# Kernel optimization log

Measured on AMD Instinct MI355X. Metric: run time of the kernel, lower is better.

Reference implementation:

```python
import jax, jax.numpy as jnp
import numpy as np

B, C, T = 8, 512, 4096
KC, VC, H = 512, 512, 1  # key_channels, value_channels, num_heads
SCALE = KC // (H ** 0.5)  # faithful to original: key_channels // num_heads**0.5


def setup_inputs() -> dict:
    key = jax.random.key(0)
    k1, k2, k3, k4, k5 = jax.random.split(key, 5)
    x = jax.random.normal(k1, (B, C, T), dtype=jnp.float32)
    # 1x1 Conv1d weights: Conv1d(C, out, kernel_size=1) == per-timestep Linear
    Wqk = jax.random.normal(k2, (KC, C), dtype=jnp.float32) / np.sqrt(C)
    bqk = jax.random.normal(k3, (KC,), dtype=jnp.float32) * 0.01
    Wv = jax.random.normal(k4, (VC, C), dtype=jnp.float32) / np.sqrt(C)
    bv = jax.random.normal(k5, (VC,), dtype=jnp.float32) * 0.01
    return {"x": x, "Wqk": Wqk, "bqk": bqk, "Wv": Wv, "bv": bv}


def reference(x, Wqk, bqk, Wv, bv):
    # 1x1 conv projections: [B,C,T] -> [B,K,T] / [B,V,T]
    qk = jnp.einsum('kc,bct->bkt', Wqk, x) + bqk[None, :, None]
    val = jnp.einsum('vc,bct->bvt', Wv, x) + bv[None, :, None]
    # channel-wise attention: with num_heads=1 the reshape/transpose/matmul
    # chain reduces to scores[b,k,v] = sum_t qk[b,k,t] * val[b,v,t]
    scores = jnp.einsum('bkt,bvt->bkv', qk, val) / SCALE
    p = jax.nn.softmax(scores, axis=-1)          # softmax over value channels
    # inference path: dropout is identity (self.training == False)
    out = jnp.einsum('bkv,bvt->bkt', p, val)     # [B,K,T], K == input_channels
    return out.reshape(-1, C, T)
```

## Files before the change

kernel.cpp:

```cpp
#include <hip/hip_runtime.h>
#include <hip/hip_bf16.h>


#define BB 8
#define CC 512
#define TT 4096

typedef __attribute__((ext_vector_type(8))) short bf16x8;
typedef __attribute__((ext_vector_type(4))) short bf16x4;
typedef __attribute__((ext_vector_type(4))) float f32x4;

__device__ __forceinline__ void gload_lds16(const void* g, void* l) {
  __builtin_amdgcn_global_load_lds((const __attribute__((address_space(1))) void*)g,
                                   (__attribute__((address_space(3))) void*)l,
                                   16, 0, 0);
}
__device__ __forceinline__ float bf2f(short u) {
  return __uint_as_float(((unsigned)(unsigned short)u) << 16);
}
__device__ __forceinline__ unsigned short f2bf(float f) {
  return __builtin_bit_cast(unsigned short, __float2bfloat16(f));
}
__device__ __forceinline__ void bar_fence() {
  asm volatile("" ::: "memory");
  __builtin_amdgcn_s_barrier();
  asm volatile("" ::: "memory");
}
__device__ __forceinline__ void bar_lds() {
  asm volatile("s_waitcnt lgkmcnt(0)" ::: "memory");
  __builtin_amdgcn_s_barrier();
  asm volatile("" ::: "memory");
}

__global__ __launch_bounds__(256)
void convert_stream_kernel(const float* __restrict__ x, __hip_bfloat16* __restrict__ xh,
                           float* __restrict__ sx)
{
  const int gid = blockIdx.x * 256 + threadIdx.x;
#pragma unroll
  for (int it = 0; it < 4; it++) {
    const int chunk = it * 524288 + gid;
    const size_t base = (size_t)chunk * 8;
    const float4 a = *(const float4*)&x[base];
    const float4 c = *(const float4*)&x[base + 4];
    bf16x8 h;
    h[0] = (short)f2bf(a.x); h[1] = (short)f2bf(a.y);
    h[2] = (short)f2bf(a.z); h[3] = (short)f2bf(a.w);
    h[4] = (short)f2bf(c.x); h[5] = (short)f2bf(c.y);
    h[6] = (short)f2bf(c.z); h[7] = (short)f2bf(c.w);
    *(bf16x8*)&xh[base] = h;
    float s = ((a.x + a.y) + (a.z + a.w)) + ((c.x + c.y) + (c.z + c.w));
#pragma unroll
    for (int off = 32; off; off >>= 1) s += __shfl_xor(s, off);
    if ((threadIdx.x & 63) == 0) atomicAdd(&sx[chunk >> 9], s);
  }
}

__global__ __launch_bounds__(256)
void prep_w_kernel(const float* __restrict__ Wqk, const float* __restrict__ Wv,
                   const float* __restrict__ sx,
                   __hip_bfloat16* __restrict__ Wqkh, __hip_bfloat16* __restrict__ Wvh,
                   __hip_bfloat16* __restrict__ WvT,
                   float* __restrict__ ta, float* __restrict__ tb)
{
  const int blk = blockIdx.x;
  if (blk < 1024) {
    int i = blk * 256 + threadIdx.x;
    Wqkh[i] = __float2bfloat16(Wqk[i]);
    float wv = Wv[i];
    Wvh[i] = __float2bfloat16(wv);
    WvT[(i & 511) * 512 + (i >> 9)] = __float2bfloat16(wv);
  } else {
    int wid = threadIdx.x >> 6, lane = threadIdx.x & 63;
    int gid = (blk - 1024) * 4 + wid;
    int which = gid >> 12;
    int rem = gid & 4095;
    int b = rem >> 9, j = rem & 511;
    const float* W = which ? Wv : Wqk;
    float s = 0.f;
#pragma unroll
    for (int i2 = 0; i2 < 8; i2++) {
      int c = lane + i2 * 64;
      s += W[j * 512 + c] * sx[b * 512 + c];
    }
#pragma unroll
    for (int off = 32; off; off >>= 1) s += __shfl_xor(s, off);
    if (lane == 0) (which ? tb : ta)[b * 512 + j] = s;
  }
}

template <int BM, int BN>
__global__ __launch_bounds__(256)
void gemm_nt_kernel(const __hip_bfloat16* __restrict__ A, long strideA, int ldA,
                    const __hip_bfloat16* __restrict__ B, long strideB, int ldB,
                    void* __restrict__ C, long strideC, int ldC,
                    int Kslice, int nslices)
{
  static_assert(BM == 128 && BN == 128, "vmcnt(8) count assumes 8 loads/stage");
  constexpr int FM = BM / 32, FN = BN / 32;
  const int tid = threadIdx.x, lane = tid & 63, wid = tid >> 6;

  const int gx = gridDim.x, gy = gridDim.y;
  const int lin = blockIdx.x + gx * (blockIdx.y + gy * blockIdx.z);
  const int nwg = gx * gy * (int)gridDim.z;
  const int lin2 = (lin & 7) * (nwg >> 3) + (lin >> 3);
  const int tn = lin2 % gx;
  const int r1 = lin2 / gx;
  const int tm = r1 % gy;
  const int z  = r1 / gy;
  const int b  = z / nslices;
  const int ks = z - b * nslices;

  const __hip_bfloat16* Ab = A + (size_t)b * strideA + (size_t)(tm * BM) * ldA + (size_t)ks * Kslice;
  const __hip_bfloat16* Bb = B + (size_t)b * strideB + (size_t)(tn * BN) * ldB + (size_t)ks * Kslice;

  __shared__ __align__(16) __hip_bfloat16 sA[2][BM * 64];
  __shared__ __align__(16) __hip_bfloat16 sB[2][BN * 64];

  const int wr = wid >> 1, wc = wid & 1;

  f32x4 acc[FM][FN];
#pragma unroll
  for (int m = 0; m < FM; m++)
#pragma unroll
    for (int n = 0; n < FN; n++) acc[m][n] = (f32x4){0.f, 0.f, 0.f, 0.f};

  auto stage = [&](int buf, int k0) {
#pragma unroll
    for (int i = 0; i < BM / 32; i++) {
      int e = tid * 8 + i * 2048;
      int row = e >> 6, colg = (e & 63) ^ ((row & 7) << 3);
      gload_lds16(Ab + (size_t)row * ldA + k0 + colg, &sA[buf][wid * 512 + i * 2048]);
    }
#pragma unroll
    for (int i = 0; i < BN / 32; i++) {
      int e = tid * 8 + i * 2048;
      int row = e >> 6, colg = (e & 63) ^ ((row & 7) << 3);
      gload_lds16(Bb + (size_t)row * ldB + k0 + colg, &sB[buf][wid * 512 + i * 2048]);
    }
  };

  const int nsteps = Kslice >> 6;
  stage(0, 0);
  if (nsteps > 1) stage(1, 64);
#pragma unroll 1
  for (int s = 0; s < nsteps; s++) {
    if (s + 1 < nsteps) asm volatile("s_waitcnt vmcnt(8)" ::: "memory");
    else                asm volatile("s_waitcnt vmcnt(0)" ::: "memory");
    bar_fence();
    const __hip_bfloat16* cA = sA[s & 1];
    const __hip_bfloat16* cB = sB[s & 1];
#pragma unroll
    for (int ks2 = 0; ks2 < 2; ks2++) {
      bf16x8 af[FM], bfv[FN];
      const int kb = ks2 * 32 + (lane >> 4) * 8;
#pragma unroll
      for (int m = 0; m < FM; m++) {
        int row = wr * (BM / 2) + m * 16 + (lane & 15);
        af[m] = *(const bf16x8*)&cA[row * 64 + (kb ^ ((row & 7) << 3))];
      }
#pragma unroll
      for (int n = 0; n < FN; n++) {
        int row = wc * (BN / 2) + n * 16 + (lane & 15);
        bfv[n] = *(const bf16x8*)&cB[row * 64 + (kb ^ ((row & 7) << 3))];
      }
#pragma unroll
      for (int m = 0; m < FM; m++)
#pragma unroll
        for (int n = 0; n < FN; n++)
          acc[m][n] = __builtin_amdgcn_mfma_f32_16x16x32_bf16(af[m], bfv[n], acc[m][n], 0, 0, 0);
    }
    bar_fence();
    if (s + 2 < nsteps) stage(s & 1, (s + 2) << 6);
  }

  const int rb = tm * BM + wr * (BM / 2) + ((lane >> 4) << 2);
  const int cb = tn * BN + wc * (BN / 2) + (lane & 15);
  __hip_bfloat16* Cb = (__hip_bfloat16*)C + (size_t)z * strideC;
#pragma unroll
  for (int m = 0; m < FM; m++)
#pragma unroll
    for (int n = 0; n < FN; n++)
#pragma unroll
      for (int r = 0; r < 4; r++) {
        int row = rb + m * 16 + r, col = cb + n * 16;
        Cb[(size_t)row * ldC + col] = __float2bfloat16(acc[m][n][r]);
      }
}

__global__ __launch_bounds__(256)
void reduce_g_kernel(const short* __restrict__ Gpart, short* __restrict__ Gb)
{
  const int idx = (blockIdx.x * 256 + threadIdx.x) * 8;
  const int b = idx >> 18, i = idx & 262143;
  const short* base = Gpart + ((size_t)(b * 4) << 18) + i;
  float s[8];
#pragma unroll
  for (int q = 0; q < 8; q++) s[q] = 0.f;
#pragma unroll
  for (int ks = 0; ks < 4; ks++) {
    bf16x8 v = *(const bf16x8*)(base + ((size_t)ks << 18));
#pragma unroll
    for (int q = 0; q < 8; q++) s[q] += bf2f(v[q]);
  }
  bf16x8 o;
#pragma unroll
  for (int q = 0; q < 8; q++) o[q] = (short)f2bf(s[q]);
  *(bf16x8*)(Gb + ((size_t)b << 18) + i) = o;
}

__global__ __launch_bounds__(256)
void middle_kernel(const __hip_bfloat16* __restrict__ Gh,
                   const __hip_bfloat16* __restrict__ Wqkh,
                   const __hip_bfloat16* __restrict__ Wvh,
                   const __hip_bfloat16* __restrict__ WvT,
                   const float* __restrict__ bqk, const float* __restrict__ bv,
                   const float* __restrict__ ta, const float* __restrict__ tb,
                   __hip_bfloat16* __restrict__ Mm, float* __restrict__ pb)
{
  __shared__ __align__(16) __hip_bfloat16 sW[16 * 512];
  __shared__ __align__(16) __hip_bfloat16 sT[16 * 512];
  __shared__ __align__(16) __hip_bfloat16 sB[2][512 * 32];
  __shared__ float red1[4][16], red2[4][16], red3[4][16];

  const int tid = threadIdx.x, lane = tid & 63, wid = tid >> 6;
  const int lin = blockIdx.x;
  const int lin2 = (lin & 7) * 32 + (lin >> 3);
  const int strip = lin2 & 31, b = lin2 >> 5;
  const __hip_bfloat16* Ghb = Gh + (size_t)b * 262144;

#pragma unroll
  for (int i = 0; i < 4; i++) {
    int row = i * 4 + wid;
    int scol = 8 * (lane ^ (row & 7));
    gload_lds16(Wqkh + (size_t)(strip * 16 + row) * 512 + scol, &sW[i * 2048 + wid * 512]);
  }

  auto stageB = [&](int buf, int gt) {
    const __hip_bfloat16* Bsrc = (gt < 16) ? Ghb : (gt < 32 ? Wvh : WvT);
    const int k0 = (gt & 15) * 32;
#pragma unroll
    for (int i = 0; i < 8; i++) {
      int r = i * 64 + wid * 16 + (lane >> 2);
      int scol = k0 + 8 * ((lane & 3) ^ ((r >> 1) & 3));
      gload_lds16(Bsrc + (size_t)r * 512 + scol, &sB[buf][i * 2048 + wid * 512]);
    }
  };

  stageB(0, 0);
  stageB(1, 1);

  const int arow = lane & 15;
  const int asw = (arow & 7) << 3;
  const int kb = (lane >> 4) * 8;
  f32x4 acc[8];

  auto run16 = [&](int base, const __hip_bfloat16* SX) {
#pragma unroll
    for (int n = 0; n < 8; n++) acc[n] = (f32x4){0.f, 0.f, 0.f, 0.f};
#pragma unroll 1
    for (int t = 0; t < 16; t++) {
      const int gt = base + t;
      if (gt + 1 < 48) asm volatile("s_waitcnt vmcnt(8)" ::: "memory");
      else             asm volatile("s_waitcnt vmcnt(0)" ::: "memory");
      bar_fence();
      const __hip_bfloat16* cB = sB[gt & 1];
      const int kq = t * 32 + kb;
      bf16x8 af = *(const bf16x8*)&SX[arow * 512 + (kq ^ asw)];
#pragma unroll
      for (int n = 0; n < 8; n++) {
        int brow = wid * 128 + n * 16 + (lane & 15);
        bf16x8 bfv = *(const bf16x8*)&cB[brow * 32 + (kb ^ (((brow >> 1) & 3) << 3))];
        acc[n] = __builtin_amdgcn_mfma_f32_16x16x32_bf16(af, bfv, acc[n], 0, 0, 0);
      }
      bar_fence();
      if (gt + 2 < 48) stageB(gt & 1, gt + 2);
    }
  };

  run16(0, sW);
#pragma unroll
  for (int n = 0; n < 8; n++)
#pragma unroll
    for (int r = 0; r < 4; r++) {
      int lr = ((lane >> 4) << 2) + r;
      int col = wid * 128 + n * 16 + (lane & 15);
      sT[lr * 512 + (col ^ ((lr & 7) << 3))] = __float2bfloat16(acc[n][r]);
    }
  bar_lds();

  run16(16, sT);

  const float* tab = ta + b * 512;
  const float* tbb = tb + b * 512;
  float bvc[8], tbc[8];
#pragma unroll
  for (int n = 0; n < 8; n++) {
    int col = wid * 128 + n * 16 + (lane & 15);
    bvc[n] = bv[col]; tbc[n] = tbb[col];
  }
  float bq[4], tar[4];
#pragma unroll
  for (int r = 0; r < 4; r++) {
    int gr = strip * 16 + ((lane >> 4) << 2) + r;
    bq[r] = bqk[gr]; tar[r] = tab[gr];
  }
#pragma unroll
  for (int n = 0; n < 8; n++)
#pragma unroll
    for (int r = 0; r < 4; r++)
      acc[n][r] = (acc[n][r] + bq[r] * tbc[n] + tar[r] * bvc[n]
                   + 4096.0f * bq[r] * bvc[n]) * (1.0f / 512.0f);

#pragma unroll
  for (int r = 0; r < 4; r++) {
    float v = acc[0][r];
#pragma unroll
    for (int n = 1; n < 8; n++) v = fmaxf(v, acc[n][r]);
#pragma unroll
    for (int off = 1; off < 16; off <<= 1) v = fmaxf(v, __shfl_xor(v, off));
    if ((lane & 15) == 0) red1[wid][((lane >> 4) << 2) + r] = v;
  }
  bar_lds();
  float mx[4];
#pragma unroll
  for (int r = 0; r < 4; r++) {
    int lr = ((lane >> 4) << 2) + r;
    mx[r] = fmaxf(fmaxf(red1[0][lr], red1[1][lr]), fmaxf(red1[2][lr], red1[3][lr]));
  }
#pragma unroll
  for (int r = 0; r < 4; r++) {
    float s = 0.f, pp = 0.f;
#pragma unroll
    for (int n = 0; n < 8; n++) {
      float e = __expf(acc[n][r] - mx[r]);
      acc[n][r] = e;
      s += e; pp += e * bvc[n];
    }
#pragma unroll
    for (int off = 1; off < 16; off <<= 1) { s += __shfl_xor(s, off); pp += __shfl_xor(pp, off); }
    if ((lane & 15) == 0) {
      red2[wid][((lane >> 4) << 2) + r] = s;
      red3[wid][((lane >> 4) << 2) + r] = pp;
    }
  }
  bar_lds();
  float inv[4];
#pragma unroll
  for (int r = 0; r < 4; r++) {
    int lr = ((lane >> 4) << 2) + r;
    float sum = red2[0][lr] + red2[1][lr] + red2[2][lr] + red2[3][lr];
    inv[r] = 1.0f / sum;
    if (wid == 0 && (lane & 15) == 0)
      pb[b * 512 + strip * 16 + lr] =
          (red3[0][lr] + red3[1][lr] + red3[2][lr] + red3[3][lr]) * inv[r];
  }
#pragma unroll
  for (int n = 0; n < 8; n++)
#pragma unroll
    for (int r = 0; r < 4; r++) {
      int lr = ((lane >> 4) << 2) + r;
      int col = wid * 128 + n * 16 + (lane & 15);
      sT[lr * 512 + (col ^ ((lr & 7) << 3))] = __float2bfloat16(acc[n][r] * inv[r]);
    }
  bar_lds();

  run16(32, sT);

  __hip_bfloat16* Mb = Mm + (size_t)b * 262144 + (size_t)(strip * 16) * 512;
#pragma unroll
  for (int n = 0; n < 8; n++)
#pragma unroll
    for (int r = 0; r < 4; r++) {
      int lr = ((lane >> 4) << 2) + r;
      int col = wid * 128 + n * 16 + (lane & 15);
      Mb[(size_t)lr * 512 + col] = __float2bfloat16(acc[n][r]);
    }
}

__global__ __launch_bounds__(256)
void gemm_out_kernel(const __hip_bfloat16* __restrict__ Mall,
                     const __hip_bfloat16* __restrict__ xh,
                     const float* __restrict__ pball,
                     float* __restrict__ out)
{
  __shared__ __align__(16) __hip_bfloat16 sA[2][128 * 64];
  __shared__ __align__(16) __hip_bfloat16 sB[2][64 * 128];

  const int tid = threadIdx.x, lane = tid & 63, wid = tid >> 6;
  const int wr = wid >> 1, wc = wid & 1;

  const int lin = blockIdx.x + 32 * (blockIdx.y + 4 * blockIdx.z);
  const int lin2 = (lin & 7) * 128 + (lin >> 3);
  const int tm = lin2 & 3;
  const int tn = (lin2 >> 2) & 31;
  const int b  = lin2 >> 7;

  const __hip_bfloat16* Ab = Mall + (size_t)b * 262144 + (size_t)(tm * 128) * 512;
  const __hip_bfloat16* Bb = xh + (size_t)b * ((size_t)CC * TT) + tn * 128;

  f32x4 acc[4][4];
#pragma unroll
  for (int m = 0; m < 4; m++)
#pragma unroll
    for (int n = 0; n < 4; n++) acc[m][n] = (f32x4){0.f, 0.f, 0.f, 0.f};

  auto stage = [&](int buf, int k0) {
#pragma unroll
    for (int i = 0; i < 4; i++) {
      int e = tid * 8 + i * 2048;
      int row = e >> 6, colg = (e & 63) ^ ((row & 7) << 3);
      gload_lds16(Ab + (size_t)row * 512 + k0 + colg, &sA[buf][wid * 512 + i * 2048]);
    }
#pragma unroll
    for (int q = 0; q < 4; q++) {
      int E = q * 2048 + tid * 8;
      int v = ((E >> 9) << 2) | ((E >> 4) & 3);
      int t = (((E >> 6) & 7) << 4) | (E & 8);
      gload_lds16(Bb + (size_t)(k0 + v) * TT + t, &sB[buf][wid * 512 + q * 2048]);
    }
  };

  const unsigned sB32 =
      (unsigned)(size_t)(__attribute__((address_space(3))) __hip_bfloat16*)&sB[0][0];
  const unsigned btr_lo = sB32 + (lane >> 4) * 2048 + (lane & 15) * 8 + wc * 512;
  const unsigned btr_hi = btr_lo + 8192;

#define COMPUTE(BUF)                                                            \
  {                                                                             \
    _Pragma("unroll")                                                           \
    for (int ks2 = 0; ks2 < 2; ks2++) {                                         \
      bf16x8 af[4]; bf16x4 blo[4], bhi[4];                                      \
      const int kb = ks2 * 32 + (lane >> 4) * 8;                                \
      _Pragma("unroll")                                                         \
      for (int m = 0; m < 4; m++) {                                             \
        int row = wr * 64 + m * 16 + (lane & 15);                               \
        af[m] = *(const bf16x8*)&sA[BUF][row * 64 + (kb ^ ((row & 7) << 3))];   \
      }                                                                         \
      unsigned ab = ks2 ? btr_hi : btr_lo;                                      \
      _Pragma("unroll")                                                         \
      for (int n = 0; n < 4; n++) {                                             \
        asm volatile("ds_read_b64_tr_b16 %0, %1 offset:%2"                      \
                     : "=v"(blo[n]) : "v"(ab), "i"((BUF) * 16384 + n * 128));   \
        asm volatile("ds_read_b64_tr_b16 %0, %1 offset:%2"                      \
                     : "=v"(bhi[n]) : "v"(ab), "i"((BUF) * 16384 + n * 128 + 1024)); \
      }                                                                         \
      asm volatile("s_waitcnt lgkmcnt(0)" ::: "memory");                        \
      __builtin_amdgcn_sched_barrier(0);                                        \
      _Pragma("unroll")                                                         \
      for (int m = 0; m < 4; m++)                                               \
        _Pragma("unroll")                                                       \
        for (int n = 0; n < 4; n++) {                                           \
          bf16x8 b8 = __builtin_shufflevector(blo[n], bhi[n], 0, 1, 2, 3, 4, 5, 6, 7); \
          acc[m][n] = __builtin_amdgcn_mfma_f32_16x16x32_bf16(af[m], b8, acc[m][n], 0, 0, 0); \
        }                                                                       \
    }                                                                           \
  }

  stage(0, 0);
  stage(1, 64);
#pragma unroll 1
  for (int s = 0; s < 8; s += 2) {
    asm volatile("s_waitcnt vmcnt(8)" ::: "memory");
    bar_fence();
    COMPUTE(0);
    bar_fence();
    if (s + 2 < 8) stage(0, (s + 2) * 64);
    if (s + 2 < 8) asm volatile("s_waitcnt vmcnt(8)" ::: "memory");
    else           asm volatile("s_waitcnt vmcnt(0)" ::: "memory");
    bar_fence();
    COMPUTE(1);
    bar_fence();
    if (s + 3 < 8) stage(1, (s + 3) * 64);
  }
#undef COMPUTE

  const int rb = tm * 128 + wr * 64 + ((lane >> 4) << 2);
  const int cb = tn * 128 + wc * 64 + (lane & 15);
  float* Cf = out + (size_t)b * ((size_t)CC * TT);
  const float* pbv = pball + b * 512;
#pragma unroll
  for (int m = 0; m < 4; m++)
#pragma unroll
    for (int n = 0; n < 4; n++)
#pragma unroll
      for (int r = 0; r < 4; r++) {
        int row = rb + m * 16 + r, col = cb + n * 16;
        Cf[(size_t)row * TT + col] = acc[m][n][r] + pbv[row];
      }
}

extern "C" void kernel_launch(void* const* d_in, const int* in_sizes, int n_in,
                              void* d_out, int out_size, void* d_ws, size_t ws_size,
                              hipStream_t stream)
{
  const float* x   = (const float*)d_in[0];
  const float* Wqk = (const float*)d_in[1];
  const float* bqk = (const float*)d_in[2];
  const float* Wv  = (const float*)d_in[3];
  const float* bv  = (const float*)d_in[4];
  float* out = (float*)d_out;

  char* w = (char*)d_ws;
  auto alloc = [&](size_t bytes) {
    void* pp = (void*)w;
    w += (bytes + 255) & ~(size_t)255;
    return pp;
  };
  __hip_bfloat16* xh     = (__hip_bfloat16*)alloc((size_t)BB * CC * TT * 2);
  short*          Gpart  = (short*)alloc((size_t)BB * 4 * CC * CC * 2);
  short*          Gb     = (short*)alloc((size_t)BB * CC * CC * 2);
  __hip_bfloat16* Mm     = (__hip_bfloat16*)alloc((size_t)BB * CC * CC * 2);
  __hip_bfloat16* Wqkh   = (__hip_bfloat16*)alloc((size_t)CC * CC * 2);
  __hip_bfloat16* Wvh    = (__hip_bfloat16*)alloc((size_t)CC * CC * 2);
  __hip_bfloat16* WvT    = (__hip_bfloat16*)alloc((size_t)CC * CC * 2);
  float* sx = (float*)alloc((size_t)BB * CC * 4);
  float* ta = (float*)alloc((size_t)BB * CC * 4);
  float* tb = (float*)alloc((size_t)BB * CC * 4);
  float* pb = (float*)alloc((size_t)BB * CC * 4);

  hipMemsetAsync(sx, 0, (size_t)BB * CC * 4, stream);

  convert_stream_kernel<<<2048, 256, 0, stream>>>(x, xh, sx);
  prep_w_kernel<<<3072, 256, 0, stream>>>(Wqk, Wv, sx, Wqkh, Wvh, WvT, ta, tb);

  const long sXH = (long)CC * TT;
  const long sSq = (long)CC * CC;

  gemm_nt_kernel<128, 128><<<dim3(4, 4, BB * 4), 256, 0, stream>>>(
      xh, sXH, TT, xh, sXH, TT, Gpart, sSq, CC, 1024, 4);
  reduce_g_kernel<<<(BB * CC * CC) / (256 * 8), 256, 0, stream>>>(Gpart, Gb);

  middle_kernel<<<256, 256, 0, stream>>>(
      (const __hip_bfloat16*)Gb, Wqkh, Wvh, WvT, bqk, bv, ta, tb, Mm, pb);

  gemm_out_kernel<<<dim3(32, 4, 8), 256, 0, stream>>>(Mm, xh, pb, out);
}
```

Before: 215.7 us.

## Double split-K for Gram GEMM and read middle-kernel operands directly from global

```diff
diff --git a/kernel.cpp b/kernel.cpp
--- a/kernel.cpp
+++ b/kernel.cpp
@@ -193,12 +193,12 @@
 {
   const int idx = (blockIdx.x * 256 + threadIdx.x) * 8;
   const int b = idx >> 18, i = idx & 262143;
-  const short* base = Gpart + ((size_t)(b * 4) << 18) + i;
+  const short* base = Gpart + ((size_t)(b * 8) << 18) + i;
   float s[8];
 #pragma unroll
   for (int q = 0; q < 8; q++) s[q] = 0.f;
 #pragma unroll
-  for (int ks = 0; ks < 4; ks++) {
+  for (int ks = 0; ks < 8; ks++) {
     bf16x8 v = *(const bf16x8*)(base + ((size_t)ks << 18));
 #pragma unroll
     for (int q = 0; q < 8; q++) s[q] += bf2f(v[q]);
@@ -218,9 +218,7 @@
                    const float* __restrict__ ta, const float* __restrict__ tb,
                    __hip_bfloat16* __restrict__ Mm, float* __restrict__ pb)
 {
-  __shared__ __align__(16) __hip_bfloat16 sW[16 * 512];
   __shared__ __align__(16) __hip_bfloat16 sT[16 * 512];
-  __shared__ __align__(16) __hip_bfloat16 sB[2][512 * 32];
   __shared__ float red1[4][16], red2[4][16], red3[4][16];
 
   const int tid = threadIdx.x, lane = tid & 63, wid = tid >> 6;
@@ -229,56 +227,27 @@
   const int strip = lin2 & 31, b = lin2 >> 5;
   const __hip_bfloat16* Ghb = Gh + (size_t)b * 262144;
 
-#pragma unroll
-  for (int i = 0; i < 4; i++) {
-    int row = i * 4 + wid;
-    int scol = 8 * (lane ^ (row & 7));
-    gload_lds16(Wqkh + (size_t)(strip * 16 + row) * 512 + scol, &sW[i * 2048 + wid * 512]);
-  }
-
-  auto stageB = [&](int buf, int gt) {
-    const __hip_bfloat16* Bsrc = (gt < 16) ? Ghb : (gt < 32 ? Wvh : WvT);
-    const int k0 = (gt & 15) * 32;
-#pragma unroll
-    for (int i = 0; i < 8; i++) {
-      int r = i * 64 + wid * 16 + (lane >> 2);
-      int scol = k0 + 8 * ((lane & 3) ^ ((r >> 1) & 3));
-      gload_lds16(Bsrc + (size_t)r * 512 + scol, &sB[buf][i * 2048 + wid * 512]);
-    }
-  };
-
-  stageB(0, 0);
-  stageB(1, 1);
-
   const int arow = lane & 15;
   const int asw = (arow & 7) << 3;
   const int kb = (lane >> 4) * 8;
+  const size_t browK = (size_t)(wid * 128 + (lane & 15)) * 512;
   f32x4 acc[8];
 
-  auto run16 = [&](int base, const __hip_bfloat16* SX) {
-#pragma unroll
-    for (int n = 0; n < 8; n++) acc[n] = (f32x4){0.f, 0.f, 0.f, 0.f};
-#pragma unroll 1
-    for (int t = 0; t < 16; t++) {
-      const int gt = base + t;
-      if (gt + 1 < 48) asm volatile("s_waitcnt vmcnt(8)" ::: "memory");
-      else             asm volatile("s_waitcnt vmcnt(0)" ::: "memory");
-      bar_fence();
-      const __hip_bfloat16* cB = sB[gt & 1];
-      const int kq = t * 32 + kb;
-      bf16x8 af = *(const bf16x8*)&SX[arow * 512 + (kq ^ asw)];
-#pragma unroll
-      for (int n = 0; n < 8; n++) {
-        int brow = wid * 128 + n * 16 + (lane & 15);
-        bf16x8 bfv = *(const bf16x8*)&cB[brow * 32 + (kb ^ (((brow >> 1) & 3) << 3))];
-        acc[n] = __builtin_amdgcn_mfma_f32_16x16x32_bf16(af, bfv, acc[n], 0, 0, 0);
-      }
-      bar_fence();
-      if (gt + 2 < 48) stageB(gt & 1, gt + 2);
-    }
-  };
-
-  run16(0, sW);
+#define RUN16(AF_EXPR, BSRC)                                                    \
+  {                                                                             \
+    _Pragma("unroll") for (int n = 0; n < 8; n++) acc[n] = (f32x4){0.f,0.f,0.f,0.f}; \
+    _Pragma("unroll") for (int t = 0; t < 16; t++) {                            \
+      const int kq = t * 32 + kb;                                               \
+      bf16x8 af = (AF_EXPR);                                                    \
+      _Pragma("unroll") for (int n = 0; n < 8; n++) {                           \
+        bf16x8 bfv = *(const bf16x8*)&(BSRC)[browK + (size_t)n * 16 * 512 + kq];\
+        acc[n] = __builtin_amdgcn_mfma_f32_16x16x32_bf16(af, bfv, acc[n], 0, 0, 0); \
+      }                                                                         \
+    }                                                                           \
+  }
+
+  const __hip_bfloat16* Aq = Wqkh + (size_t)(strip * 16 + arow) * 512;
+  RUN16(*(const bf16x8*)&Aq[kq], Ghb);
 #pragma unroll
   for (int n = 0; n < 8; n++)
 #pragma unroll
@@ -289,7 +258,7 @@
     }
   bar_lds();
 
-  run16(16, sT);
+  RUN16(*(const bf16x8*)&sT[arow * 512 + (kq ^ asw)], Wvh);
 
   const float* tab = ta + b * 512;
   const float* tbb = tb + b * 512;
@@ -365,7 +334,8 @@
     }
   bar_lds();
 
-  run16(32, sT);
+  RUN16(*(const bf16x8*)&sT[arow * 512 + (kq ^ asw)], WvT);
+#undef RUN16
 
   __hip_bfloat16* Mb = Mm + (size_t)b * 262144 + (size_t)(strip * 16) * 512;
 #pragma unroll
@@ -508,7 +478,7 @@
     return pp;
   };
   __hip_bfloat16* xh     = (__hip_bfloat16*)alloc((size_t)BB * CC * TT * 2);
-  short*          Gpart  = (short*)alloc((size_t)BB * 4 * CC * CC * 2);
+  short*          Gpart  = (short*)alloc((size_t)BB * 8 * CC * CC * 2);
   short*          Gb     = (short*)alloc((size_t)BB * CC * CC * 2);
   __hip_bfloat16* Mm     = (__hip_bfloat16*)alloc((size_t)BB * CC * CC * 2);
   __hip_bfloat16* Wqkh   = (__hip_bfloat16*)alloc((size_t)CC * CC * 2);
@@ -527,8 +497,8 @@
   const long sXH = (long)CC * TT;
   const long sSq = (long)CC * CC;
 
-  gemm_nt_kernel<128, 128><<<dim3(4, 4, BB * 4), 256, 0, stream>>>(
-      xh, sXH, TT, xh, sXH, TT, Gpart, sSq, CC, 1024, 4);
+  gemm_nt_kernel<128, 128><<<dim3(4, 4, BB * 8), 256, 0, stream>>>(
+      xh, sXH, TT, xh, sXH, TT, Gpart, sSq, CC, 512, 8);
   reduce_g_kernel<<<(BB * CC * CC) / (256 * 8), 256, 0, stream>>>(Gpart, Gb);
 
   middle_kernel<<<256, 256, 0, stream>>>(
```

Result: slower. 231.8 us (+7.4%).
